# Kernel optimization log

Hardware: AMD Instinct MI355X
Metric: run time of the kernel (lower is better)

The kernel has to match this reference:

```python
import jax, jax.numpy as jnp
import numpy as np

V, D, H, B, LK, LQ, PAD = 10000, 300, 512, 16, 64, 64, 0


def _lstm(x, Wih, Whh, b, h0, c0):
    # x: [B,T,D]; Wih: [4G,D]; Whh: [4G,G]; b: [4G] (b_ih+b_hh); torch gate order i,f,g,o
    xg = jnp.einsum('btd,gd->btg', x, Wih) + b
    def step(hc, xt):
        h, c = hc
        g = xt + h @ Whh.T
        i, f, gg, o = jnp.split(g, 4, axis=-1)
        c = jax.nn.sigmoid(f) * c + jax.nn.sigmoid(i) * jnp.tanh(gg)
        h = jax.nn.sigmoid(o) * jnp.tanh(c)
        return (h, c), h
    (hT, cT), hs = jax.lax.scan(step, (h0, c0), jnp.swapaxes(xg, 0, 1))
    return jnp.swapaxes(hs, 0, 1), hT, cT


def setup_inputs() -> dict:
    key = jax.random.key(0)
    ks = jax.random.split(key, 24)
    n = lambda k, s: (jax.random.normal(k, s, jnp.float32) * 0.05)
    return {
        'source': jax.random.randint(ks[0], (B, LK), 0, V),
        'prev_outputs': jax.random.randint(ks[1], (B, LQ), 0, V),
        'emb': n(ks[2], (V, D)),
        'enc_f_Wih': n(ks[3], (4 * H, D)), 'enc_f_Whh': n(ks[4], (4 * H, H)), 'enc_f_b': n(ks[5], (4 * H,)),
        'enc_b_Wih': n(ks[6], (4 * H, D)), 'enc_b_Whh': n(ks[7], (4 * H, H)), 'enc_b_b': n(ks[8], (4 * H,)),
        'dec_Wih': n(ks[9], (8 * H, D)), 'dec_Whh': n(ks[10], (8 * H, 2 * H)), 'dec_b': n(ks[11], (8 * H,)),
        'k_W': n(ks[12], (2 * H, 2 * H)), 'k_b': n(ks[13], (2 * H,)),
        'v_W': n(ks[14], (2 * H, 2 * H)), 'v_b': n(ks[15], (2 * H,)),
        'fc1_W': n(ks[16], (2 * H, 4 * H)), 'fc1_b': n(ks[17], (2 * H,)),
        'fc2_W': n(ks[18], (V, 2 * H)), 'fc2_b': n(ks[19], (V,)),
    }


def reference(source, prev_outputs, emb, enc_f_Wih, enc_f_Whh, enc_f_b,
              enc_b_Wih, enc_b_Whh, enc_b_b, dec_Wih, dec_Whh, dec_b,
              k_W, k_b, v_W, v_b, fc1_W, fc1_b, fc2_W, fc2_b):
    bsz = source.shape[0]
    xs = emb[source]  # [B,LK,300]
    z = jnp.zeros((bsz, H), xs.dtype)
    out_f, hf, cf = _lstm(xs, enc_f_Wih, enc_f_Whh, enc_f_b, z, z)
    out_b, hb, cb = _lstm(xs[:, ::-1], enc_b_Wih, enc_b_Whh, enc_b_b, z, z)
    enc_out = jnp.concatenate([out_f, out_b[:, ::-1]], axis=-1)  # [B,LK,1024]
    # self.change: interleave fwd/bwd channels -> [B,1024]
    h0 = jnp.stack([hf, hb], axis=-1).reshape(bsz, 2 * H)
    c0 = jnp.stack([cf, cb], axis=-1).reshape(bsz, 2 * H)
    Q, _, _ = _lstm(emb[prev_outputs], dec_Wih, dec_Whh, dec_b, h0, c0)  # [B,LQ,1024]
    K = enc_out @ k_W.T + k_b
    Vv = enc_out @ v_W.T + v_b
    M = jnp.einsum('bqc,bkc->bqk', Q, K)
    mask = (source == PAD)[:, None, :]
    M = jnp.where(mask, -jnp.inf, M)
    A = jax.nn.softmax(M, axis=2)
    ctx = jnp.einsum('bqk,bkc->bqc', A, Vv)  # == (A[...,None]*V[:,None]).sum(2)
    x = jnp.tanh(jnp.concatenate([ctx, Q], axis=-1) @ fc1_W.T + fc1_b)  # dropout=identity (eval)
    return x @ fc2_W.T + fc2_b
```

## Files before the change

### kernel.cpp

```cpp
#include <hip/hip_runtime.h>
#include <cmath>

#define BB   16
#define LKK  64
#define LQQ  64
#define DD   300
#define HH   512
#define H2   1024
#define G4   2048
#define G8   4096
#define VV   10000

__device__ __forceinline__ float sigmoidf_(float x) { return 1.f / (1.f + expf(-x)); }

typedef __attribute__((ext_vector_type(4))) float    f4_;
typedef __attribute__((ext_vector_type(4))) unsigned u4_;

__device__ __forceinline__ float ld_sc(const float* p) {
    return __hip_atomic_load(p, __ATOMIC_RELAXED, __HIP_MEMORY_SCOPE_AGENT);
}
__device__ __forceinline__ void st_sc(float* p, float v) {
    __hip_atomic_store(p, v, __ATOMIC_RELAXED, __HIP_MEMORY_SCOPE_AGENT);
}

__device__ __forceinline__ f4_ ld4_sc(const float* p) {
    f4_ r;
    asm volatile("global_load_dwordx4 %0, %1, off sc0 sc1" : "=v"(r) : "v"(p));
    return r;
}
__device__ __forceinline__ u4_ ld4u_sc(const unsigned* p) {
    u4_ r;
    asm volatile("global_load_dwordx4 %0, %1, off sc0 sc1" : "=v"(r) : "v"(p));
    return r;
}
__device__ __forceinline__ void wait_vm0() {
    asm volatile("s_waitcnt vmcnt(0)" ::: "memory");
    __builtin_amdgcn_sched_barrier(0);
}

__device__ __forceinline__ void gbar2(unsigned* flags, int wg, unsigned target) {
    asm volatile("s_waitcnt vmcnt(0)" ::: "memory");
    if (threadIdx.x == 0)
        __hip_atomic_store(&flags[wg], target, __ATOMIC_RELAXED, __HIP_MEMORY_SCOPE_AGENT);
    if (threadIdx.x < 64) {
        for (;;) {
            u4_ f = ld4u_sc(flags + (threadIdx.x << 2));
            wait_vm0();
            unsigned m0 = f[0] < f[1] ? f[0] : f[1];
            unsigned m1 = f[2] < f[3] ? f[2] : f[3];
            unsigned mn = m0 < m1 ? m0 : m1;
            if (__all((int)(mn >= target))) break;
            __builtin_amdgcn_s_sleep(1);
        }
    }
    __syncthreads();
}

__global__ void rev_idx_kernel(const int* __restrict__ src, int* __restrict__ rev,
                               unsigned* __restrict__ bars) {
    int tid = blockIdx.x * blockDim.x + threadIdx.x;
    if (tid < 512) bars[tid] = 0u;
    if (tid < BB * LKK) {
        int b = tid / LKK, t = tid % LKK;
        rev[tid] = src[b * LKK + (LKK - 1 - t)];
    }
}

typedef __attribute__((ext_vector_type(8))) short bfrag8;
typedef __attribute__((ext_vector_type(4))) float facc4;

__device__ __forceinline__ unsigned short f2bf(float x) {
    unsigned u = __float_as_uint(x);
    unsigned r = (u + 0x7fffu + ((u >> 16) & 1u)) >> 16;
    return (unsigned short)r;
}

#define ASTR 40

__global__ __launch_bounds__(256)
void gemm_mfma128(const float* __restrict__ A, const int* __restrict__ gidx, int lda,
                  const float* __restrict__ Bw, int ldb,
                  const float* __restrict__ bias,
                  float* __restrict__ C, int ldc,
                  int N, int K, int act) {
    __shared__ __align__(16) short Ah[128 * ASTR];
    __shared__ __align__(16) short Al[128 * ASTR];
    __shared__ __align__(16) short Bh[128 * ASTR];
    __shared__ __align__(16) short Bl[128 * ASTR];
    int m0 = blockIdx.x * 128;
    int n0 = blockIdx.y * 128;
    int tid = threadIdx.x;
    int lane = tid & 63, w = tid >> 6;
    int wr = w >> 1, wc = w & 1;
    int fr = lane & 15, fg = lane >> 4;

    int sr = tid >> 1, sc = (tid & 1) << 4;
    long abase = gidx ? (long)gidx[m0 + sr] * lda : (long)(m0 + sr) * lda;
    int gn = n0 + sr;
    bool bval = gn < N;
    long bbase = (long)gn * ldb;

    facc4 acc[4][4] = {};

    for (int k0 = 0; k0 < K; k0 += 32) {
        {
            float v[16];
            if (k0 + sc + 16 <= K) {
                const float* ap = A + abase + k0 + sc;
                float4 t0 = *(const float4*)(ap + 0);
                float4 t1 = *(const float4*)(ap + 4);
                float4 t2 = *(const float4*)(ap + 8);
                float4 t3 = *(const float4*)(ap + 12);
                v[0]=t0.x; v[1]=t0.y; v[2]=t0.z;  v[3]=t0.w;
                v[4]=t1.x; v[5]=t1.y; v[6]=t1.z;  v[7]=t1.w;
                v[8]=t2.x; v[9]=t2.y; v[10]=t2.z; v[11]=t2.w;
                v[12]=t3.x; v[13]=t3.y; v[14]=t3.z; v[15]=t3.w;
            } else {
#pragma unroll
                for (int c = 0; c < 16; c++) {
                    int k = k0 + sc + c;
                    v[c] = (k < K) ? A[abase + k] : 0.f;
                }
            }
            bfrag8 h0, h1, l0, l1;
#pragma unroll
            for (int c = 0; c < 8; c++) {
                unsigned short hb = f2bf(v[c]);
                float hf = __uint_as_float(((unsigned)hb) << 16);
                h0[c] = (short)hb; l0[c] = (short)f2bf(v[c] - hf);
            }
#pragma unroll
            for (int c = 0; c < 8; c++) {
                unsigned short hb = f2bf(v[8 + c]);
                float hf = __uint_as_float(((unsigned)hb) << 16);
                h1[c] = (short)hb; l1[c] = (short)f2bf(v[8 + c] - hf);
            }
            *(bfrag8*)&Ah[sr * ASTR + sc]     = h0;
            *(bfrag8*)&Ah[sr * ASTR + sc + 8] = h1;
            *(bfrag8*)&Al[sr * ASTR + sc]     = l0;
            *(bfrag8*)&Al[sr * ASTR + sc + 8] = l1;
        }
        {
            float v[16];
            if (bval && (k0 + sc + 16 <= K)) {
                const float* bp = Bw + bbase + k0 + sc;
                float4 t0 = *(const float4*)(bp + 0);
                float4 t1 = *(const float4*)(bp + 4);
                float4 t2 = *(const float4*)(bp + 8);
                float4 t3 = *(const float4*)(bp + 12);
                v[0]=t0.x; v[1]=t0.y; v[2]=t0.z;  v[3]=t0.w;
                v[4]=t1.x; v[5]=t1.y; v[6]=t1.z;  v[7]=t1.w;
                v[8]=t2.x; v[9]=t2.y; v[10]=t2.z; v[11]=t2.w;
                v[12]=t3.x; v[13]=t3.y; v[14]=t3.z; v[15]=t3.w;
            } else {
#pragma unroll
                for (int c = 0; c < 16; c++) {
                    int k = k0 + sc + c;
                    v[c] = (bval && k < K) ? Bw[bbase + k] : 0.f;
                }
            }
            bfrag8 h0, h1, l0, l1;
#pragma unroll
            for (int c = 0; c < 8; c++) {
                unsigned short hb = f2bf(v[c]);
                float hf = __uint_as_float(((unsigned)hb) << 16);
                h0[c] = (short)hb; l0[c] = (short)f2bf(v[c] - hf);
            }
#pragma unroll
            for (int c = 0; c < 8; c++) {
                unsigned short hb = f2bf(v[8 + c]);
                float hf = __uint_as_float(((unsigned)hb) << 16);
                h1[c] = (short)hb; l1[c] = (short)f2bf(v[8 + c] - hf);
            }
            *(bfrag8*)&Bh[sr * ASTR + sc]     = h0;
            *(bfrag8*)&Bh[sr * ASTR + sc + 8] = h1;
            *(bfrag8*)&Bl[sr * ASTR + sc]     = l0;
            *(bfrag8*)&Bl[sr * ASTR + sc + 8] = l1;
        }
        __syncthreads();

        bfrag8 ah[4], al[4], bh[4], bl[4];
#pragma unroll
        for (int i = 0; i < 4; i++) {
            int ar = wr * 64 + i * 16 + fr;
            ah[i] = *(const bfrag8*)&Ah[ar * ASTR + fg * 8];
            al[i] = *(const bfrag8*)&Al[ar * ASTR + fg * 8];
            int br = wc * 64 + i * 16 + fr;
            bh[i] = *(const bfrag8*)&Bh[br * ASTR + fg * 8];
            bl[i] = *(const bfrag8*)&Bl[br * ASTR + fg * 8];
        }
#pragma unroll
        for (int i = 0; i < 4; i++)
#pragma unroll
            for (int j = 0; j < 4; j++) {
                acc[i][j] = __builtin_amdgcn_mfma_f32_16x16x32_bf16(ah[i], bh[j], acc[i][j], 0, 0, 0);
                acc[i][j] = __builtin_amdgcn_mfma_f32_16x16x32_bf16(ah[i], bl[j], acc[i][j], 0, 0, 0);
                acc[i][j] = __builtin_amdgcn_mfma_f32_16x16x32_bf16(al[i], bh[j], acc[i][j], 0, 0, 0);
            }
        __syncthreads();
    }

#pragma unroll
    for (int i = 0; i < 4; i++) {
        int row = m0 + wr * 64 + i * 16 + fg * 4;
#pragma unroll
        for (int j = 0; j < 4; j++) {
            int col = n0 + wc * 64 + j * 16 + fr;
            if (col < N) {
                float bz = bias[col];
#pragma unroll
                for (int q = 0; q < 4; q++) {
                    float vv = acc[i][j][q] + bz;
                    if (act == 1) vv = tanhf(vv);
                    C[(long)(row + q) * ldc + col] = vv;
                }
            }
        }
    }
}

__global__ __launch_bounds__(256, 1)
void enc_recur(const float* __restrict__ xg_f, const float* __restrict__ xg_b,
               const float* __restrict__ Wf, const float* __restrict__ Wb,
               float* __restrict__ hglob, float* __restrict__ enc_out,
               float* __restrict__ encc, unsigned* __restrict__ flags) {
    __shared__ float hs[HH * 16];
    __shared__ float gbuf[BB * 17];
    int wg  = blockIdx.x;
    int dir = wg >> 7;
    int j0  = (wg & 127) * 4;
    int tid = threadIdx.x;
    int ks   = tid & 31;
    int tile = tid >> 5;
    int bh   = tile >> 2;
    int nql  = (tile & 3) << 2;
    int gate = nql >> 2;
    int sw   = (ks >> 2) & 3;
    const float* W  = dir ? Wb : Wf;
    const float* xg = dir ? xg_b : xg_f;

    float wreg[4][16];
#pragma unroll
    for (int jn = 0; jn < 4; jn++) {
        const float* wrow = W + (long)(gate * HH + j0 + jn) * HH;
#pragma unroll
        for (int j = 0; j < 16; j++) wreg[jn][j] = wrow[ks + 32 * j];
    }

    int ub = tid & 15, ujj = tid >> 4;
    float creg = 0.f;
    float4* hsv = (float4*)hs;

    for (int t = 0; t < LKK; t++) {
        if (t == 0) {
            for (int i = tid; i < HH * 16; i += 256) hs[i] = 0.f;
        } else {
            const float* hg = hglob + (long)((dir << 1) | (t & 1)) * (HH * 16);
            f4_ vv[8];
#pragma unroll
            for (int u = 0; u < 8; u++) vv[u] = ld4_sc(hg + tid * 4 + u * 1024);
            wait_vm0();
#pragma unroll
            for (int u = 0; u < 8; u++) {
                int e = tid * 4 + u * 1024;
                int jj = e >> 4, b0 = e & 15;
                *(f4_*)&hs[(jj << 4) + ((((b0 >> 2) ^ ((jj >> 2) & 3))) << 2)] = vv[u];
            }
        }
        float4 xr[8];
        if (ks == 0) {
#pragma unroll
            for (int i = 0; i < 8; i++) {
                const float* xp = xg + (long)((bh * 8 + i) * LKK + t) * G4 + gate * HH + j0;
                xr[i] = *(const float4*)xp;
            }
        }
        __syncthreads();

        float acc[8][4];
#pragma unroll
        for (int i = 0; i < 8; i++)
#pragma unroll
            for (int jn = 0; jn < 4; jn++) acc[i][jn] = 0.f;
#pragma unroll
        for (int j = 0; j < 16; j++) {
            int k = ks + 32 * j;
            float4 h0 = hsv[k * 4 + ((bh * 2 + 0) ^ sw)];
            float4 h1 = hsv[k * 4 + ((bh * 2 + 1) ^ sw)];
#pragma unroll
            for (int jn = 0; jn < 4; jn++) {
                float w = wreg[jn][j];
                acc[0][jn] += h0.x * w; acc[1][jn] += h0.y * w;
                acc[2][jn] += h0.z * w; acc[3][jn] += h0.w * w;
                acc[4][jn] += h1.x * w; acc[5][jn] += h1.y * w;
                acc[6][jn] += h1.z * w; acc[7][jn] += h1.w * w;
            }
        }
#pragma unroll
        for (int i = 0; i < 8; i++)
#pragma unroll
            for (int jn = 0; jn < 4; jn++) {
                float v = acc[i][jn];
                v += __shfl_xor(v, 1, 64);  v += __shfl_xor(v, 2, 64);
                v += __shfl_xor(v, 4, 64);  v += __shfl_xor(v, 8, 64);
                v += __shfl_xor(v, 16, 64);
                acc[i][jn] = v;
            }
        if (ks == 0) {
#pragma unroll
            for (int i = 0; i < 8; i++)
#pragma unroll
                for (int jn = 0; jn < 4; jn++)
                    gbuf[(bh * 8 + i) * 17 + nql + jn] = acc[i][jn] + ((const float*)&xr[i])[jn];
        }
        __syncthreads();

        if (tid < 64) {
            int j = j0 + ujj;
            float gi = gbuf[ub * 17 + 0  + ujj];
            float gf = gbuf[ub * 17 + 4  + ujj];
            float gg = gbuf[ub * 17 + 8  + ujj];
            float go = gbuf[ub * 17 + 12 + ujj];
            float cv = sigmoidf_(gf) * creg + sigmoidf_(gi) * tanhf(gg);
            creg = cv;
            float hv = sigmoidf_(go) * tanhf(cv);
            st_sc(&hglob[(long)((dir << 1) | ((t + 1) & 1)) * (HH * 16) + j * 16 + ub], hv);
            int kpos = dir ? (LKK - 1 - t) : t;
            enc_out[(long)(ub * LKK + kpos) * H2 + dir * HH + j] = hv;
            if (t == LKK - 1) encc[(dir * BB + ub) * HH + j] = creg;
        }
        if (t < LKK - 1) gbar2(flags, wg, (unsigned)(t + 1));
    }
}

__global__ __launch_bounds__(256, 1)
void dec_recur(const float* __restrict__ xg_d, const float* __restrict__ Wd,
               const float* __restrict__ enc_out, const float* __restrict__ encc,
               float* __restrict__ hglob, float* __restrict__ Qout,
               unsigned* __restrict__ flags) {
    __shared__ float hs[HH * 16];
    __shared__ float gbuf[BB * 17];
    int wg  = blockIdx.x;
    int j0  = wg * 4;
    int tid = threadIdx.x;
    int ks   = tid & 31;
    int tile = tid >> 5;
    int bh   = tile >> 2;
    int nql  = (tile & 3) << 2;
    int gate = nql >> 2;
    int sw   = (ks >> 2) & 3;

    float wreg[4][32];
#pragma unroll
    for (int jn = 0; jn < 4; jn++) {
        const float* wrow = Wd + (long)(gate * H2 + j0 + jn) * H2;
#pragma unroll
        for (int j = 0; j < 32; j++) wreg[jn][j] = wrow[ks + 32 * j];
    }

    int ub = tid & 15, ujj = tid >> 4;
    float creg = 0.f;
    if (tid < 64) {
        int j = j0 + ujj;
        creg = ((j & 1) == 0) ? encc[ub * HH + (j >> 1)]
                              : encc[(BB + ub) * HH + (j >> 1)];
    }
    float4* hsv = (float4*)hs;

    for (int t = 0; t < LQQ; t++) {
        float4 xr[8];
        if (ks == 0) {
#pragma unroll
            for (int i = 0; i < 8; i++) {
                const float* xp = xg_d + (long)((bh * 8 + i) * LQQ + t) * G8 + gate * H2 + j0;
                xr[i] = *(const float4*)xp;
            }
        }
        float acc[8][4];
#pragma unroll
        for (int i = 0; i < 8; i++)
#pragma unroll
            for (int jn = 0; jn < 4; jn++) acc[i][jn] = 0.f;

        auto do_fma = [&](int half) {
#pragma unroll
            for (int jj2 = 0; jj2 < 16; jj2++) {
                int j = half * 16 + jj2;
                int kl = ks + 32 * jj2;
                float4 h0 = hsv[kl * 4 + ((bh * 2 + 0) ^ sw)];
                float4 h1 = hsv[kl * 4 + ((bh * 2 + 1) ^ sw)];
#pragma unroll
                for (int jn = 0; jn < 4; jn++) {
                    float w = wreg[jn][j];
                    acc[0][jn] += h0.x * w; acc[1][jn] += h0.y * w;
                    acc[2][jn] += h0.z * w; acc[3][jn] += h0.w * w;
                    acc[4][jn] += h1.x * w; acc[5][jn] += h1.y * w;
                    acc[6][jn] += h1.z * w; acc[7][jn] += h1.w * w;
                }
            }
        };

        if (t == 0) {
            for (int half = 0; half < 2; half++) {
                for (int e = tid; e < HH * 16; e += 256) {
                    int kl = e >> 4, b = e & 15;
                    int k = half * HH + kl;
                    float hv = ((k & 1) == 0)
                        ? enc_out[(long)(b * LKK + (LKK - 1)) * H2 + (k >> 1)]
                        : enc_out[(long)(b * LKK) * H2 + HH + (k >> 1)];
                    hs[(kl << 4) + ((((b >> 2) ^ ((kl >> 2) & 3))) << 2) + (b & 3)] = hv;
                }
                __syncthreads();
                do_fma(half);
                __syncthreads();
            }
        } else {
            const float* hgA = hglob + (long)(t & 1) * (H2 * 16);
            f4_ vvA[8], vvB[8];
#pragma unroll
            for (int u = 0; u < 8; u++) vvA[u] = ld4_sc(hgA + tid * 4 + u * 1024);
            wait_vm0();
#pragma unroll
            for (int u = 0; u < 8; u++) {
                int e = tid * 4 + u * 1024;
                int kl = e >> 4, b0 = e & 15;
                *(f4_*)&hs[(kl << 4) + ((((b0 >> 2) ^ ((kl >> 2) & 3))) << 2)] = vvA[u];
            }
#pragma unroll
            for (int u = 0; u < 8; u++) vvB[u] = ld4_sc(hgA + (HH * 16) + tid * 4 + u * 1024);
            __syncthreads();
            do_fma(0);
            __syncthreads();
            wait_vm0();
#pragma unroll
            for (int u = 0; u < 8; u++) {
                int e = tid * 4 + u * 1024;
                int kl = e >> 4, b0 = e & 15;
                *(f4_*)&hs[(kl << 4) + ((((b0 >> 2) ^ ((kl >> 2) & 3))) << 2)] = vvB[u];
            }
            __syncthreads();
            do_fma(1);
            __syncthreads();
        }

#pragma unroll
        for (int i = 0; i < 8; i++)
#pragma unroll
            for (int jn = 0; jn < 4; jn++) {
                float v = acc[i][jn];
                v += __shfl_xor(v, 1, 64);  v += __shfl_xor(v, 2, 64);
                v += __shfl_xor(v, 4, 64);  v += __shfl_xor(v, 8, 64);
                v += __shfl_xor(v, 16, 64);
                acc[i][jn] = v;
            }
        if (ks == 0) {
#pragma unroll
            for (int i = 0; i < 8; i++)
#pragma unroll
                for (int jn = 0; jn < 4; jn++)
                    gbuf[(bh * 8 + i) * 17 + nql + jn] = acc[i][jn] + ((const float*)&xr[i])[jn];
        }
        __syncthreads();

        if (tid < 64) {
            int j = j0 + ujj;
            float gi = gbuf[ub * 17 + 0  + ujj];
            float gf = gbuf[ub * 17 + 4  + ujj];
            float gg = gbuf[ub * 17 + 8  + ujj];
            float go = gbuf[ub * 17 + 12 + ujj];
            float cv = sigmoidf_(gf) * creg + sigmoidf_(gi) * tanhf(gg);
            creg = cv;
            float hv = sigmoidf_(go) * tanhf(cv);
            st_sc(&hglob[(long)((t + 1) & 1) * (H2 * 16) + j * 16 + ub], hv);
            Qout[(long)(ub * LQQ + t) * H2 + j] = hv;
        }
        if (t < LQQ - 1) gbar2(flags, wg, (unsigned)(t + 1));
    }
}

__global__ __launch_bounds__(256)
void attention_kernel(const float* __restrict__ Qm, const float* __restrict__ Km,
                      const float* __restrict__ Vm, const int* __restrict__ source,
                      float* __restrict__ concatBuf) {
    int b = blockIdx.x >> 6;
    int q = blockIdx.x & 63;
    int tid = threadIdx.x;
    __shared__ float qrow[H2];
    __shared__ float part[LKK][4];
    __shared__ float aw[LKK];

    for (int i = tid; i < H2; i += 256) qrow[i] = Qm[(long)(b * LQQ + q) * H2 + i];
    __syncthreads();

    int k = tid >> 2, p = tid & 3;
    {
        const float* krow = Km + (long)(b * LKK + k) * H2 + p * 256;
        const float* qp = qrow + p * 256;
        float s = 0.f;
#pragma unroll 4
        for (int i = 0; i < 256; i++) s += qp[i] * krow[i];
        part[k][p] = s;
    }
    __syncthreads();
    if (tid < 64) {
        float sc = part[tid][0] + part[tid][1] + part[tid][2] + part[tid][3];
        bool masked = (source[b * LKK + tid] == 0);
        float m = masked ? -INFINITY : sc;
#pragma unroll
        for (int o = 32; o >= 1; o >>= 1) m = fmaxf(m, __shfl_xor(m, o, 64));
        float e = masked ? 0.f : expf(sc - m);
        float sum = e;
#pragma unroll
        for (int o = 32; o >= 1; o >>= 1) sum += __shfl_xor(sum, o, 64);
        aw[tid] = e / sum;
    }
    __syncthreads();

    for (int c = tid; c < H2; c += 256) {
        float acc = 0.f;
#pragma unroll 8
        for (int kk = 0; kk < LKK; kk++) acc += aw[kk] * Vm[(long)(b * LKK + kk) * H2 + c];
        long row = (long)(b * LQQ + q) * (2 * H2);
        concatBuf[row + c] = acc;
        concatBuf[row + H2 + c] = qrow[c];
    }
}

extern "C" void kernel_launch(void* const* d_in, const int* in_sizes, int n_in,
                              void* d_out, int out_size, void* d_ws, size_t ws_size,
                              hipStream_t stream) {
    const int*   src       = (const int*)  d_in[0];
    const int*   prev      = (const int*)  d_in[1];
    const float* emb       = (const float*)d_in[2];
    const float* enc_f_Wih = (const float*)d_in[3];
    const float* enc_f_Whh = (const float*)d_in[4];
    const float* enc_f_b   = (const float*)d_in[5];
    const float* enc_b_Wih = (const float*)d_in[6];
    const float* enc_b_Whh = (const float*)d_in[7];
    const float* enc_b_b   = (const float*)d_in[8];
    const float* dec_Wih   = (const float*)d_in[9];
    const float* dec_Whh   = (const float*)d_in[10];
    const float* dec_b     = (const float*)d_in[11];
    const float* k_W  = (const float*)d_in[12];
    const float* k_b  = (const float*)d_in[13];
    const float* v_W  = (const float*)d_in[14];
    const float* v_b  = (const float*)d_in[15];
    const float* fc1_W = (const float*)d_in[16];
    const float* fc1_b = (const float*)d_in[17];
    const float* fc2_W = (const float*)d_in[18];
    const float* fc2_b = (const float*)d_in[19];
    float* out = (float*)d_out;

    float* p = (float*)d_ws;
    float* xg_f    = p; p += (long)BB * LKK * G4;
    float* xg_b    = p; p += (long)BB * LKK * G4;
    float* xg_d    = p; p += (long)BB * LQQ * G8;
    float* enc_out = p; p += (long)BB * LKK * H2;
    float* encc    = p; p += 2L * BB * HH;
    float* hg_enc  = p; p += 2L * 2 * HH * 16;
    float* hg_dec  = p; p += 2L * H2 * 16;
    float* Qbuf    = p; p += (long)BB * LQQ * H2;
    float* Kbuf    = p; p += (long)BB * LKK * H2;
    float* Vbuf    = p; p += (long)BB * LKK * H2;
    float* concatB = p; p += (long)BB * LQQ * 2 * H2;
    float* fc1out  = p; p += (long)BB * LQQ * H2;
    int*   rev     = (int*)p; p += (BB * LKK);
    unsigned* bars = (unsigned*)p; p += 512;

    rev_idx_kernel<<<4, 256, 0, stream>>>(src, rev, bars);

    gemm_mfma128<<<dim3(8, G4 / 128), 256, 0, stream>>>(emb, src, DD, enc_f_Wih, DD,
                                                        enc_f_b, xg_f, G4, G4, DD, 0);
    gemm_mfma128<<<dim3(8, G4 / 128), 256, 0, stream>>>(emb, rev, DD, enc_b_Wih, DD,
                                                        enc_b_b, xg_b, G4, G4, DD, 0);
    gemm_mfma128<<<dim3(8, G8 / 128), 256, 0, stream>>>(emb, prev, DD, dec_Wih, DD,
                                                        dec_b, xg_d, G8, G8, DD, 0);

    enc_recur<<<dim3(256), dim3(256), 0, stream>>>(xg_f, xg_b, enc_f_Whh, enc_b_Whh,
                                                   hg_enc, enc_out, encc, bars);

    gemm_mfma128<<<dim3(8, 8), 256, 0, stream>>>(enc_out, nullptr, H2, k_W, H2,
                                                 k_b, Kbuf, H2, H2, H2, 0);
    gemm_mfma128<<<dim3(8, 8), 256, 0, stream>>>(enc_out, nullptr, H2, v_W, H2,
                                                 v_b, Vbuf, H2, H2, H2, 0);

    dec_recur<<<dim3(256), dim3(256), 0, stream>>>(xg_d, dec_Whh, enc_out, encc,
                                                   hg_dec, Qbuf, bars + 256);

    attention_kernel<<<BB * LQQ, 256, 0, stream>>>(Qbuf, Kbuf, Vbuf, src, concatB);

    gemm_mfma128<<<dim3(8, 8), 256, 0, stream>>>(concatB, nullptr, 2 * H2, fc1_W, 2 * H2,
                                                 fc1_b, fc1out, H2, H2, 2 * H2, 1);

    gemm_mfma128<<<dim3(8, (VV + 127) / 128), 256, 0, stream>>>(fc1out, nullptr, H2, fc2_W, H2,
                                                                fc2_b, out, VV, VV, H2, 0);
}
```

Baseline: 1.868 ms.

## Replace shuffle reductions with LDS transpose reduction and batch GEMM launches

In both LSTM recurrence kernels, the 5-step cross-lane shuffle reduction per gate accumulator is replaced by writing partial sums to a padded shared-memory buffer. All 256 threads then each reduce one row, and every thread loads its single xg input element instead of lane 0 loading eight float4s. One trailing __syncthreads in the decoder inner loop is removed. Separately, the three input-projection GEMMs and the K/V GEMMs are merged into single launches through a shared gemm_core device function. This cuts per-step serial latency and launch count, at the cost of about 33 KB extra LDS per block and an extra barrier per step.

```diff
diff --git a/kernel.cpp b/kernel.cpp
--- a/kernel.cpp
+++ b/kernel.cpp
@@ -16,9 +16,6 @@
 typedef __attribute__((ext_vector_type(4))) float    f4_;
 typedef __attribute__((ext_vector_type(4))) unsigned u4_;
 
-__device__ __forceinline__ float ld_sc(const float* p) {
-    return __hip_atomic_load(p, __ATOMIC_RELAXED, __HIP_MEMORY_SCOPE_AGENT);
-}
 __device__ __forceinline__ void st_sc(float* p, float v) {
     __hip_atomic_store(p, v, __ATOMIC_RELAXED, __HIP_MEMORY_SCOPE_AGENT);
 }
@@ -77,18 +74,14 @@
 
 #define ASTR 40
 
-__global__ __launch_bounds__(256)
-void gemm_mfma128(const float* __restrict__ A, const int* __restrict__ gidx, int lda,
-                  const float* __restrict__ Bw, int ldb,
-                  const float* __restrict__ bias,
-                  float* __restrict__ C, int ldc,
-                  int N, int K, int act) {
-    __shared__ __align__(16) short Ah[128 * ASTR];
-    __shared__ __align__(16) short Al[128 * ASTR];
-    __shared__ __align__(16) short Bh[128 * ASTR];
-    __shared__ __align__(16) short Bl[128 * ASTR];
-    int m0 = blockIdx.x * 128;
-    int n0 = blockIdx.y * 128;
+__device__ __forceinline__ void gemm_core(
+        short* __restrict__ Ah, short* __restrict__ Al,
+        short* __restrict__ Bh, short* __restrict__ Bl,
+        const float* __restrict__ A, const int* __restrict__ gidx, int lda,
+        const float* __restrict__ Bw, int ldb,
+        const float* __restrict__ bias,
+        float* __restrict__ C, int ldc,
+        int N, int K, int act, int m0, int n0) {
     int tid = threadIdx.x;
     int lane = tid & 63, w = tid >> 6;
     int wr = w >> 1, wc = w & 1;
@@ -219,13 +212,71 @@
     }
 }
 
+__global__ __launch_bounds__(256)
+void gemm_mfma128(const float* __restrict__ A, const int* __restrict__ gidx, int lda,
+                  const float* __restrict__ Bw, int ldb,
+                  const float* __restrict__ bias,
+                  float* __restrict__ C, int ldc,
+                  int N, int K, int act) {
+    __shared__ __align__(16) short Ah[128 * ASTR];
+    __shared__ __align__(16) short Al[128 * ASTR];
+    __shared__ __align__(16) short Bh[128 * ASTR];
+    __shared__ __align__(16) short Bl[128 * ASTR];
+    gemm_core(Ah, Al, Bh, Bl, A, gidx, lda, Bw, ldb, bias, C, ldc, N, K, act,
+              blockIdx.x * 128, blockIdx.y * 128);
+}
+
+__global__ __launch_bounds__(256)
+void gemm_kv(const float* __restrict__ enc_out,
+             const float* __restrict__ kW, const float* __restrict__ kb,
+             const float* __restrict__ vW, const float* __restrict__ vb,
+             float* __restrict__ Kbuf, float* __restrict__ Vbuf) {
+    __shared__ __align__(16) short Ah[128 * ASTR];
+    __shared__ __align__(16) short Al[128 * ASTR];
+    __shared__ __align__(16) short Bh[128 * ASTR];
+    __shared__ __align__(16) short Bl[128 * ASTR];
+    int ny = blockIdx.y;
+    if (ny < 8)
+        gemm_core(Ah, Al, Bh, Bl, enc_out, nullptr, H2, kW, H2, kb, Kbuf, H2,
+                  H2, H2, 0, blockIdx.x * 128, ny * 128);
+    else
+        gemm_core(Ah, Al, Bh, Bl, enc_out, nullptr, H2, vW, H2, vb, Vbuf, H2,
+                  H2, H2, 0, blockIdx.x * 128, (ny - 8) * 128);
+}
+
+__global__ __launch_bounds__(256)
+void gemm_xg(const float* __restrict__ emb,
+             const int* __restrict__ src, const int* __restrict__ rev,
+             const int* __restrict__ prev,
+             const float* __restrict__ Wf, const float* __restrict__ bf,
+             const float* __restrict__ Wb, const float* __restrict__ bb,
+             const float* __restrict__ Wd, const float* __restrict__ bd,
+             float* __restrict__ xf, float* __restrict__ xb,
+             float* __restrict__ xd) {
+    __shared__ __align__(16) short Ah[128 * ASTR];
+    __shared__ __align__(16) short Al[128 * ASTR];
+    __shared__ __align__(16) short Bh[128 * ASTR];
+    __shared__ __align__(16) short Bl[128 * ASTR];
+    int ny = blockIdx.y;
+    if (ny < 16)
+        gemm_core(Ah, Al, Bh, Bl, emb, src, DD, Wf, DD, bf, xf, G4,
+                  G4, DD, 0, blockIdx.x * 128, ny * 128);
+    else if (ny < 32)
+        gemm_core(Ah, Al, Bh, Bl, emb, rev, DD, Wb, DD, bb, xb, G4,
+                  G4, DD, 0, blockIdx.x * 128, (ny - 16) * 128);
+    else
+        gemm_core(Ah, Al, Bh, Bl, emb, prev, DD, Wd, DD, bd, xd, G8,
+                  G8, DD, 0, blockIdx.x * 128, (ny - 32) * 128);
+}
+
 __global__ __launch_bounds__(256, 1)
 void enc_recur(const float* __restrict__ xg_f, const float* __restrict__ xg_b,
                const float* __restrict__ Wf, const float* __restrict__ Wb,
                float* __restrict__ hglob, float* __restrict__ enc_out,
                float* __restrict__ encc, unsigned* __restrict__ flags) {
     __shared__ float hs[HH * 16];
-    __shared__ float gbuf[BB * 17];
+    __shared__ float red[256 * 33];
+    __shared__ float g256[256];
     int wg  = blockIdx.x;
     int dir = wg >> 7;
     int j0  = (wg & 127) * 4;
@@ -233,8 +284,7 @@
     int ks   = tid & 31;
     int tile = tid >> 5;
     int bh   = tile >> 2;
-    int nql  = (tile & 3) << 2;
-    int gate = nql >> 2;
+    int gate = tile & 3;
     int sw   = (ks >> 2) & 3;
     const float* W  = dir ? Wb : Wf;
     const float* xg = dir ? xg_b : xg_f;
@@ -248,6 +298,7 @@
     }
 
     int ub = tid & 15, ujj = tid >> 4;
+    int xb = tid >> 4, xgate = (tid >> 2) & 3, xjn = tid & 3;
     float creg = 0.f;
     float4* hsv = (float4*)hs;
 
@@ -267,14 +318,7 @@
                 *(f4_*)&hs[(jj << 4) + ((((b0 >> 2) ^ ((jj >> 2) & 3))) << 2)] = vv[u];
             }
         }
-        float4 xr[8];
-        if (ks == 0) {
-#pragma unroll
-            for (int i = 0; i < 8; i++) {
-                const float* xp = xg + (long)((bh * 8 + i) * LKK + t) * G4 + gate * HH + j0;
-                xr[i] = *(const float4*)xp;
-            }
-        }
+        float xval = xg[(long)(xb * LKK + t) * G4 + xgate * HH + j0 + xjn];
         __syncthreads();
 
         float acc[8][4];
@@ -299,28 +343,27 @@
 #pragma unroll
         for (int i = 0; i < 8; i++)
 #pragma unroll
-            for (int jn = 0; jn < 4; jn++) {
-                float v = acc[i][jn];
-                v += __shfl_xor(v, 1, 64);  v += __shfl_xor(v, 2, 64);
-                v += __shfl_xor(v, 4, 64);  v += __shfl_xor(v, 8, 64);
-                v += __shfl_xor(v, 16, 64);
-                acc[i][jn] = v;
-            }
-        if (ks == 0) {
-#pragma unroll
-            for (int i = 0; i < 8; i++)
-#pragma unroll
-                for (int jn = 0; jn < 4; jn++)
-                    gbuf[(bh * 8 + i) * 17 + nql + jn] = acc[i][jn] + ((const float*)&xr[i])[jn];
+            for (int jn = 0; jn < 4; jn++)
+                red[((bh * 8 + i) * 16 + gate * 4 + jn) * 33 + ks] = acc[i][jn];
+        __syncthreads();
+        {
+            const float* row = red + tid * 33;
+            float s0 = 0.f, s1 = 0.f, s2 = 0.f, s3 = 0.f;
+#pragma unroll
+            for (int u = 0; u < 8; u++) {
+                s0 += row[u * 4 + 0]; s1 += row[u * 4 + 1];
+                s2 += row[u * 4 + 2]; s3 += row[u * 4 + 3];
+            }
+            g256[tid] = ((s0 + s1) + (s2 + s3)) + xval;
         }
         __syncthreads();
 
         if (tid < 64) {
             int j = j0 + ujj;
-            float gi = gbuf[ub * 17 + 0  + ujj];
-            float gf = gbuf[ub * 17 + 4  + ujj];
-            float gg = gbuf[ub * 17 + 8  + ujj];
-            float go = gbuf[ub * 17 + 12 + ujj];
+            float gi = g256[ub * 16 + 0  + ujj];
+            float gf = g256[ub * 16 + 4  + ujj];
+            float gg = g256[ub * 16 + 8  + ujj];
+            float go = g256[ub * 16 + 12 + ujj];
             float cv = sigmoidf_(gf) * creg + sigmoidf_(gi) * tanhf(gg);
             creg = cv;
             float hv = sigmoidf_(go) * tanhf(cv);
@@ -339,15 +382,15 @@
                float* __restrict__ hglob, float* __restrict__ Qout,
                unsigned* __restrict__ flags) {
     __shared__ float hs[HH * 16];
-    __shared__ float gbuf[BB * 17];
+    __shared__ float red[256 * 33];
+    __shared__ float g256[256];
     int wg  = blockIdx.x;
     int j0  = wg * 4;
     int tid = threadIdx.x;
     int ks   = tid & 31;
     int tile = tid >> 5;
     int bh   = tile >> 2;
-    int nql  = (tile & 3) << 2;
-    int gate = nql >> 2;
+    int gate = tile & 3;
     int sw   = (ks >> 2) & 3;
 
     float wreg[4][32];
@@ -359,6 +402,7 @@
     }
 
     int ub = tid & 15, ujj = tid >> 4;
+    int xb = tid >> 4, xgate = (tid >> 2) & 3, xjn = tid & 3;
     float creg = 0.f;
     if (tid < 64) {
         int j = j0 + ujj;
@@ -368,14 +412,7 @@
     float4* hsv = (float4*)hs;
 
     for (int t = 0; t < LQQ; t++) {
-        float4 xr[8];
-        if (ks == 0) {
-#pragma unroll
-            for (int i = 0; i < 8; i++) {
-                const float* xp = xg_d + (long)((bh * 8 + i) * LQQ + t) * G8 + gate * H2 + j0;
-                xr[i] = *(const float4*)xp;
-            }
-        }
+        float xval = xg_d[(long)(xb * LQQ + t) * G8 + xgate * H2 + j0 + xjn];
         float acc[8][4];
 #pragma unroll
         for (int i = 0; i < 8; i++)
@@ -440,34 +477,32 @@
             }
             __syncthreads();
             do_fma(1);
-            __syncthreads();
         }
 
 #pragma unroll
         for (int i = 0; i < 8; i++)
 #pragma unroll
-            for (int jn = 0; jn < 4; jn++) {
-                float v = acc[i][jn];
-                v += __shfl_xor(v, 1, 64);  v += __shfl_xor(v, 2, 64);
-                v += __shfl_xor(v, 4, 64);  v += __shfl_xor(v, 8, 64);
-                v += __shfl_xor(v, 16, 64);
-                acc[i][jn] = v;
-            }
-        if (ks == 0) {
-#pragma unroll
-            for (int i = 0; i < 8; i++)
-#pragma unroll
-                for (int jn = 0; jn < 4; jn++)
-                    gbuf[(bh * 8 + i) * 17 + nql + jn] = acc[i][jn] + ((const float*)&xr[i])[jn];
+            for (int jn = 0; jn < 4; jn++)
+                red[((bh * 8 + i) * 16 + gate * 4 + jn) * 33 + ks] = acc[i][jn];
+        __syncthreads();
+        {
+            const float* row = red + tid * 33;
+            float s0 = 0.f, s1 = 0.f, s2 = 0.f, s3 = 0.f;
+#pragma unroll
+            for (int u = 0; u < 8; u++) {
+                s0 += row[u * 4 + 0]; s1 += row[u * 4 + 1];
+                s2 += row[u * 4 + 2]; s3 += row[u * 4 + 3];
+            }
+            g256[tid] = ((s0 + s1) + (s2 + s3)) + xval;
         }
         __syncthreads();
 
         if (tid < 64) {
             int j = j0 + ujj;
-            float gi = gbuf[ub * 17 + 0  + ujj];
-            float gf = gbuf[ub * 17 + 4  + ujj];
-            float gg = gbuf[ub * 17 + 8  + ujj];
-            float go = gbuf[ub * 17 + 12 + ujj];
+            float gi = g256[ub * 16 + 0  + ujj];
+            float gf = g256[ub * 16 + 4  + ujj];
+            float gg = g256[ub * 16 + 8  + ujj];
+            float go = g256[ub * 16 + 12 + ujj];
             float cv = sigmoidf_(gf) * creg + sigmoidf_(gi) * tanhf(gg);
             creg = cv;
             float hv = sigmoidf_(go) * tanhf(cv);
@@ -569,20 +604,16 @@
 
     rev_idx_kernel<<<4, 256, 0, stream>>>(src, rev, bars);
 
-    gemm_mfma128<<<dim3(8, G4 / 128), 256, 0, stream>>>(emb, src, DD, enc_f_Wih, DD,
-                                                        enc_f_b, xg_f, G4, G4, DD, 0);
-    gemm_mfma128<<<dim3(8, G4 / 128), 256, 0, stream>>>(emb, rev, DD, enc_b_Wih, DD,
-                                                        enc_b_b, xg_b, G4, G4, DD, 0);
-    gemm_mfma128<<<dim3(8, G8 / 128), 256, 0, stream>>>(emb, prev, DD, dec_Wih, DD,
-                                                        dec_b, xg_d, G8, G8, DD, 0);
+    gemm_xg<<<dim3(8, 64), 256, 0, stream>>>(emb, src, rev, prev,
+                                             enc_f_Wih, enc_f_b,
+                                             enc_b_Wih, enc_b_b,
+                                             dec_Wih, dec_b,
+                                             xg_f, xg_b, xg_d);
 
     enc_recur<<<dim3(256), dim3(256), 0, stream>>>(xg_f, xg_b, enc_f_Whh, enc_b_Whh,
                                                    hg_enc, enc_out, encc, bars);
 
-    gemm_mfma128<<<dim3(8, 8), 256, 0, stream>>>(enc_out, nullptr, H2, k_W, H2,
-                                                 k_b, Kbuf, H2, H2, H2, 0);
-    gemm_mfma128<<<dim3(8, 8), 256, 0, stream>>>(enc_out, nullptr, H2, v_W, H2,
-                                                 v_b, Vbuf, H2, H2, H2, 0);
+    gemm_kv<<<dim3(8, 16), 256, 0, stream>>>(enc_out, k_W, k_b, v_W, v_b, Kbuf, Vbuf);
 
     dec_recur<<<dim3(256), dim3(256), 0, stream>>>(xg_d, dec_Whh, enc_out, encc,
                                                    hg_dec, Qbuf, bars + 256);
```

After: 1.607 ms. 1.16x faster.
